# Kernel optimization log

Hardware: AMD Instinct MI355X
Metric: run time of the kernel (lower is better)

## Reference

```python
import jax, jax.numpy as jnp
from jax import lax
import numpy as np

DIM = 256
RANK = 128
E = 4      # num_experts
K = 2      # top_k
B, H, W = 8, 128, 128


def setup_inputs() -> dict:
    key = jax.random.key(0)
    ks = jax.random.split(key, 12)
    s = lambda fan: 1.0 / np.sqrt(fan)
    return {
        "x": jax.random.normal(ks[0], (B, DIM, H, W), jnp.float32),
        "shared": jax.random.normal(ks[1], (B, DIM, H, W), jnp.float32),
        # FrequencyEmbedding MLP (torch Linear: weight [out,in], bias [out])
        "mlp_w1": jax.random.normal(ks[2], (2 * DIM, DIM), jnp.float32) * s(DIM),
        "mlp_b1": jnp.zeros((2 * DIM,), jnp.float32),
        "mlp_w2": jax.random.normal(ks[3], (DIM, 2 * DIM), jnp.float32) * s(2 * DIM),
        "mlp_b2": jnp.zeros((DIM,), jnp.float32),
        # routing gates (no bias)
        "gate_w": jax.random.normal(ks[4], (E, DIM), jnp.float32) * s(DIM),
        "freq_gate_w": jax.random.normal(ks[5], (E, DIM), jnp.float32) * s(DIM),
        # stacked expert 1x1 convs: proj0/proj1 dim->rank, proj2 rank->dim
        "p0": jax.random.normal(ks[6], (E, RANK, DIM), jnp.float32) * s(DIM),
        "p1": jax.random.normal(ks[7], (E, RANK, DIM), jnp.float32) * s(DIM),
        "p2": jax.random.normal(ks[8], (E, DIM, RANK), jnp.float32) * s(RANK),
        # output 1x1 conv (no bias)
        "proj_out_w": jax.random.normal(ks[9], (DIM, DIM), jnp.float32) * s(DIM),
    }


def _high_pass_depthwise(x):
    # fixed frozen 3x3 high-pass kernel, depthwise (groups=C)
    C = x.shape[1]
    k = jnp.array([[-1., -1., -1.], [-1., 8., -1.], [-1., -1., -1.]], x.dtype)
    k = jnp.tile(k[None, None], (C, 1, 1, 1))  # [C,1,3,3]
    return lax.conv_general_dilated(
        x, k, window_strides=(1, 1), padding="SAME",
        feature_group_count=C,
        dimension_numbers=("NCHW", "OIHW", "NCHW"))


def reference(x, shared, mlp_w1, mlp_b1, mlp_w2, mlp_b2,
              gate_w, freq_gate_w, p0, p1, p2, proj_out_w):
    Bn = x.shape[0]
    # FrequencyEmbedding: high-pass conv -> GELU -> global mean -> MLP
    h = jax.nn.gelu(_high_pass_depthwise(x), approximate=False)
    h = h.mean(axis=(-2, -1))                                    # [B, C]
    freq_emb = jax.nn.gelu(h @ mlp_w1.T + mlp_b1, approximate=False) @ mlp_w2.T + mlp_b2
    # Routing: avg-pool gate + freq gate, softmax, top-k, scatter to dense gates
    pooled = x.mean(axis=(-2, -1))                               # [B, C]
    logits = pooled @ gate_w.T + freq_emb @ freq_gate_w.T        # [B, E]
    gating = jax.nn.softmax(logits, axis=-1)
    vals, idx = lax.top_k(gating, K)                             # [B, K]
    gates = jnp.zeros_like(logits).at[jnp.arange(Bn)[:, None], idx].set(vals)  # [B, E]
    a = jnp.einsum("erd,bdhw->berhw", p0, x)                     # [B,E,R,H,W]
    b = jnp.einsum("erd,bdhw->berhw", p1, shared)
    y = a * jax.nn.silu(b)
    # gate-weighted combine, folding gates into the contraction; shortcut term
    combined = (jnp.einsum("be,edr,berhw->bdhw", gates, p2, y)
                + gates.sum(-1)[:, None, None, None] * x)        # [B,C,H,W]
    out = jnp.einsum("od,bdhw->bohw", proj_out_w, combined)
    return out
```

## Files before the change

kernel.cpp:

```cpp
#include <hip/hip_runtime.h>
#include <math.h>

#define DIMC 256
#define HW   16384
#define NB   8
#define HID  512
#define NE   4
#define RNK  128

typedef __bf16 bf16x8 __attribute__((ext_vector_type(8)));
typedef float  f32x4  __attribute__((ext_vector_type(4)));

__device__ __forceinline__ unsigned short f2bf(float f) {
  unsigned u = __builtin_bit_cast(unsigned, f);
  u += 0x7FFFu + ((u >> 16) & 1u);
  return (unsigned short)(u >> 16);
}
__device__ __forceinline__ unsigned pack2(float a, float b) {
  return (unsigned)f2bf(a) | ((unsigned)f2bf(b) << 16);
}
__device__ __forceinline__ float bf2f(unsigned short u) {
  unsigned v = ((unsigned)u) << 16;
  return __builtin_bit_cast(float, v);
}

#define CPAD 136
__global__ __launch_bounds__(256) void k_conv_reduce(const float* __restrict__ x,
                                                     float* __restrict__ xsum,
                                                     float* __restrict__ hsum) {
  __shared__ unsigned short sp[128 * CPAD];
  __shared__ float red[8];
  const int p = blockIdx.x;
  const int tid = threadIdx.x;
  const float4* img4 = (const float4*)(x + (size_t)p * HW);
#pragma unroll
  for (int u = 0; u < 16; ++u) {
    const int unit = tid + 256 * u;
    const float4 v = img4[unit];
    const int row = unit >> 5, xq = unit & 31;
    uint2 w;
    w.x = pack2(v.x, v.y);
    w.y = pack2(v.z, v.w);
    *(uint2*)&sp[row * CPAD + xq * 4] = w;
  }
  __syncthreads();

  float xacc = 0.f, hacc = 0.f;
#pragma unroll
  for (int u = 0; u < 4; ++u) {
    const int seg = tid + 256 * u;
    const int row = seg >> 3, x0 = (seg & 7) * 16;
    float S[16], c[16];
#pragma unroll
    for (int j = 0; j < 16; ++j) S[j] = 0.f;
#pragma unroll
    for (int dr = -1; dr <= 1; ++dr) {
      const int r2 = row + dr;
      float v[18];
      if ((unsigned)r2 <= 127u) {
        const unsigned short* rp = sp + r2 * CPAD + x0;
        const uint4 q0 = *(const uint4*)(rp);
        const uint4 q1 = *(const uint4*)(rp + 8);
        v[0]  = (x0 > 0)       ? bf2f(rp[-1]) : 0.f;
        v[17] = (x0 + 16 < 128) ? bf2f(rp[16]) : 0.f;
        v[1] = bf2f((unsigned short)(q0.x & 0xffff)); v[2] = bf2f((unsigned short)(q0.x >> 16));
        v[3] = bf2f((unsigned short)(q0.y & 0xffff)); v[4] = bf2f((unsigned short)(q0.y >> 16));
        v[5] = bf2f((unsigned short)(q0.z & 0xffff)); v[6] = bf2f((unsigned short)(q0.z >> 16));
        v[7] = bf2f((unsigned short)(q0.w & 0xffff)); v[8] = bf2f((unsigned short)(q0.w >> 16));
        v[9]  = bf2f((unsigned short)(q1.x & 0xffff)); v[10] = bf2f((unsigned short)(q1.x >> 16));
        v[11] = bf2f((unsigned short)(q1.y & 0xffff)); v[12] = bf2f((unsigned short)(q1.y >> 16));
        v[13] = bf2f((unsigned short)(q1.z & 0xffff)); v[14] = bf2f((unsigned short)(q1.z >> 16));
        v[15] = bf2f((unsigned short)(q1.w & 0xffff)); v[16] = bf2f((unsigned short)(q1.w >> 16));
      } else {
#pragma unroll
        for (int j = 0; j < 18; ++j) v[j] = 0.f;
      }
      if (dr == 0) {
#pragma unroll
        for (int j = 0; j < 16; ++j) c[j] = v[j + 1];
      }
#pragma unroll
      for (int j = 0; j < 16; ++j) S[j] += v[j] + v[j + 1] + v[j + 2];
    }
#pragma unroll
    for (int j = 0; j < 16; ++j) {
      const float h = 9.f * c[j] - S[j];
      hacc += 0.5f * h * (1.f + erff(h * 0.70710678118654752f));
      xacc += c[j];
    }
  }
#pragma unroll
  for (int off = 32; off > 0; off >>= 1) {
    xacc += __shfl_down(xacc, off);
    hacc += __shfl_down(hacc, off);
  }
  const int wid = tid >> 6, lane = tid & 63;
  if (lane == 0) { red[wid] = xacc; red[4 + wid] = hacc; }
  __syncthreads();
  if (tid == 0) {
    xsum[p] = red[0] + red[1] + red[2] + red[3];
    hsum[p] = red[4] + red[5] + red[6] + red[7];
  }
}

__global__ __launch_bounds__(256) void k_gate_t1(
    const float* __restrict__ hsum, const float* __restrict__ w1,
    const float* __restrict__ b1, float* __restrict__ t1) {
  const int blk = blockIdx.x;
  const int b = blk >> 7;
  const int o = (blk & 127) * 4 + (threadIdx.x >> 6);
  const int lane = threadIdx.x & 63;
  const float4 h = *(const float4*)(hsum + b * DIMC + lane * 4);
  const float4 w = *(const float4*)(w1 + (size_t)o * DIMC + lane * 4);
  float acc = h.x * w.x + h.y * w.y + h.z * w.z + h.w * w.w;
#pragma unroll
  for (int off = 32; off > 0; off >>= 1) acc += __shfl_down(acc, off);
  if (lane == 0) {
    acc = acc * (1.f / 16384.f) + b1[o];
    t1[b * HID + o] = 0.5f * acc * (1.f + erff(acc * 0.70710678118654752f));
  }
}

__global__ __launch_bounds__(256) void k_gate_fe(
    const float* __restrict__ t1, const float* __restrict__ w2,
    const float* __restrict__ b2, float* __restrict__ fe) {
  const int blk = blockIdx.x;
  const int b = blk >> 6;
  const int o = (blk & 63) * 4 + (threadIdx.x >> 6);
  const int lane = threadIdx.x & 63;
  const float* tr = t1 + b * HID + lane * 8;
  const float* wr = w2 + (size_t)o * HID + lane * 8;
  const float4 ta = *(const float4*)tr,  tb = *(const float4*)(tr + 4);
  const float4 wa = *(const float4*)wr,  wb = *(const float4*)(wr + 4);
  float acc = ta.x * wa.x + ta.y * wa.y + ta.z * wa.z + ta.w * wa.w
            + tb.x * wb.x + tb.y * wb.y + tb.z * wb.z + tb.w * wb.w;
#pragma unroll
  for (int off = 32; off > 0; off >>= 1) acc += __shfl_down(acc, off);
  if (lane == 0) fe[b * DIMC + o] = acc + b2[o];
}

__global__ __launch_bounds__(256) void k_gate_fin(
    const float* __restrict__ xsum, const float* __restrict__ fe,
    const float* __restrict__ gw, const float* __restrict__ fgw,
    float* __restrict__ gates, float* __restrict__ gsumv, int* __restrict__ sel) {
  __shared__ float slog[NB][NE];
  const int wave = threadIdx.x >> 6, lane = threadIdx.x & 63;
  const int e = wave;
  const float4 g1 = *(const float4*)(gw + e * DIMC + lane * 4);
  const float4 g2 = *(const float4*)(fgw + e * DIMC + lane * 4);
  for (int b = 0; b < NB; ++b) {
    const float4 p = *(const float4*)(xsum + b * DIMC + lane * 4);
    const float4 f = *(const float4*)(fe + b * DIMC + lane * 4);
    float acc = (p.x * g1.x + p.y * g1.y + p.z * g1.z + p.w * g1.w) * (1.f / 16384.f)
              + f.x * g2.x + f.y * g2.y + f.z * g2.z + f.w * g2.w;
#pragma unroll
    for (int off = 32; off > 0; off >>= 1) acc += __shfl_down(acc, off);
    if (lane == 0) slog[b][e] = acc;
  }
  __syncthreads();
  if (threadIdx.x < NB) {
    const int b = threadIdx.x;
    float l[4] = {slog[b][0], slog[b][1], slog[b][2], slog[b][3]};
    const float m = fmaxf(fmaxf(l[0], l[1]), fmaxf(l[2], l[3]));
    float g[4];
    float ssum = 0.f;
    for (int e2 = 0; e2 < 4; ++e2) { g[e2] = expf(l[e2] - m); ssum += g[e2]; }
    for (int e2 = 0; e2 < 4; ++e2) g[e2] /= ssum;
    int i1 = 0;
    for (int e2 = 1; e2 < 4; ++e2) if (g[e2] > g[i1]) i1 = e2;
    int i2 = -1;
    for (int e2 = 0; e2 < 4; ++e2) {
      if (e2 == i1) continue;
      if (i2 < 0 || g[e2] > g[i2]) i2 = e2;
    }
    for (int e2 = 0; e2 < 4; ++e2)
      gates[b * 4 + e2] = (e2 == i1) ? g[i1] : ((e2 == i2) ? g[i2] : 0.f);
    gsumv[b] = g[i1] + g[i2];
    sel[b * 2 + 0] = i1;
    sel[b * 2 + 1] = i2;
  }
}

__global__ __launch_bounds__(128) void k_q2(const float* __restrict__ wp,
                                            const float* __restrict__ p2,
                                            float* __restrict__ q2) {
  const int eo = blockIdx.x;
  const int e = eo >> 8, o = eo & 255;
  const int r = threadIdx.x;
  const float* p2e = p2 + (size_t)e * DIMC * RNK;
  const float* wrow = wp + (size_t)o * DIMC;
  float acc = 0.f;
  for (int d = 0; d < DIMC; ++d) acc += wrow[d] * p2e[d * RNK + r];
  q2[(size_t)eo * RNK + r] = acc;
}

__global__ __launch_bounds__(256) void k_build(
    const float* __restrict__ p0, const float* __restrict__ p1,
    const float* __restrict__ wp, const float* __restrict__ q2,
    const float* __restrict__ gates, const float* __restrict__ gsumv,
    const int* __restrict__ sel,
    unsigned* __restrict__ A1u, unsigned* __restrict__ A2u,
    unsigned* __restrict__ A3u) {
  const int P1 = NB * 256 * 128;
  const int P2 = P1;
  const int P3 = NB * 256 * 256;
  for (int pi = blockIdx.x * 256 + threadIdx.x; pi < P1 + P2 + P3;
       pi += gridDim.x * 256) {
    if (pi < P1) {
      const int b = pi >> 15;
      const int row = (pi >> 7) & 255;
      const int d = (pi & 127) * 2;
      const int e = sel[b * 2 + (row >> 7)];
      const float* src = p0 + ((size_t)e * 128 + (row & 127)) * 256 + d;
      A1u[pi] = pack2(src[0], src[1]);
    } else if (pi < P1 + P2) {
      const int j = pi - P1;
      const int b = j >> 15;
      const int row = (j >> 7) & 255;
      const int d = (j & 127) * 2;
      const int e = sel[b * 2 + (row >> 7)];
      const float* src = p1 + ((size_t)e * 128 + (row & 127)) * 256 + d;
      A2u[j] = pack2(src[0], src[1]);
    } else {
      const int j = pi - P1 - P2;
      const int b = j >> 16;
      const int o = (j >> 8) & 255;
      const int c = (j & 255) * 2;
      float v0, v1;
      if (c < 256) {
        const int e = sel[b * 2 + (c >> 7)];
        const float gsc = gates[b * 4 + e];
        const float* qq = q2 + ((size_t)e * 256 + o) * RNK + (c & 127);
        v0 = gsc * qq[0]; v1 = gsc * qq[1];
      } else {
        const float gs = gsumv[b];
        const float* wr = wp + (size_t)o * DIMC + (c - 256);
        v0 = gs * wr[0]; v1 = gs * wr[1];
      }
      A3u[j] = pack2(v0, v1);
    }
  }
}

__global__ __launch_bounds__(1024, 8) void k_main_mfma(
    const float* __restrict__ x, const float* __restrict__ shr,
    const unsigned short* __restrict__ A1b, const unsigned short* __restrict__ A2b,
    const unsigned short* __restrict__ A3b, float* __restrict__ out) {
  __shared__ unsigned short XF[16384];
  __shared__ unsigned short SF[16384];
  const int tid = threadIdx.x;
  const int b = blockIdx.x & 7;
  const int tile = blockIdx.x >> 3;
  const int nb0 = tile * 64;
  const int wave = tid >> 6;
  const int lane = tid & 63;
  const int li = lane & 15;
  const int g  = lane >> 4;
  const int wrow = wave * 16;
  const size_t pbase = (size_t)b * DIMC * HW + nb0;

  {
    const int px = tid & 63;
    const int slot = tid >> 6;
#pragma unroll
    for (int pass = 0; pass < 2; ++pass) {
      const int dblk = pass * 16 + slot;
      const float* xc = x   + pbase + (size_t)(dblk * 8) * HW + px;
      const float* sc = shr + pbase + (size_t)(dblk * 8) * HW + px;
      float vx[8], vs[8];
#pragma unroll
      for (int jj = 0; jj < 8; ++jj) {
        vx[jj] = xc[(size_t)jj * HW];
        vs[jj] = sc[(size_t)jj * HW];
      }
      const int o = dblk * 512 + ((px ^ (dblk & 7)) << 3);
      uint4 wv;
      wv.x = pack2(vx[0], vx[1]); wv.y = pack2(vx[2], vx[3]);
      wv.z = pack2(vx[4], vx[5]); wv.w = pack2(vx[6], vx[7]);
      *(uint4*)&XF[o] = wv;
      uint4 sv;
      sv.x = pack2(vs[0], vs[1]); sv.y = pack2(vs[2], vs[3]);
      sv.z = pack2(vs[4], vs[5]); sv.w = pack2(vs[6], vs[7]);
      *(uint4*)&SF[o] = sv;
    }
  }
  __syncthreads();

  f32x4 accB[4], accA[4];
#pragma unroll
  for (int pb = 0; pb < 4; ++pb) { accB[pb] = (f32x4)0.f; accA[pb] = (f32x4)0.f; }
  {
    const unsigned short* Arow = A2b + ((size_t)b * 256 + wrow + li) * 256 + g * 8;
#pragma unroll
    for (int ks = 0; ks < 8; ++ks) {
      const int dblkb = ks * 4 + g;
      const int ebase = dblkb * 512 + ((li ^ (dblkb & 7)) << 3);
      const bf16x8 a0 = *(const bf16x8*)(Arow + ks * 32);
#pragma unroll
      for (int pb = 0; pb < 4; ++pb) {
        const bf16x8 bf = *(const bf16x8*)&SF[ebase + pb * 128];
        accB[pb] = __builtin_amdgcn_mfma_f32_16x16x32_bf16(a0, bf, accB[pb], 0, 0, 0);
      }
    }
  }
  {
    const unsigned short* Arow = A1b + ((size_t)b * 256 + wrow + li) * 256 + g * 8;
#pragma unroll
    for (int ks = 0; ks < 8; ++ks) {
      const int dblkb = ks * 4 + g;
      const int ebase = dblkb * 512 + ((li ^ (dblkb & 7)) << 3);
      const bf16x8 a0 = *(const bf16x8*)(Arow + ks * 32);
#pragma unroll
      for (int pb = 0; pb < 4; ++pb) {
        const bf16x8 bf = *(const bf16x8*)&XF[ebase + pb * 128];
        accA[pb] = __builtin_amdgcn_mfma_f32_16x16x32_bf16(a0, bf, accA[pb], 0, 0, 0);
      }
    }
  }
  __syncthreads();

  {
    const int ydblk = 2 * wave + (g >> 1);
    const int ys = ydblk & 7;
    const int yoff = (g & 1) * 4;
#pragma unroll
    for (int pb = 0; pb < 4; ++pb) {
      const int pxy = pb * 16 + li;
      const f32x4 aa = accA[pb], bb = accB[pb];
      const float y0 = aa[0] * (bb[0] / (1.f + __expf(-bb[0])));
      const float y1 = aa[1] * (bb[1] / (1.f + __expf(-bb[1])));
      const float y2 = aa[2] * (bb[2] / (1.f + __expf(-bb[2])));
      const float y3 = aa[3] * (bb[3] / (1.f + __expf(-bb[3])));
      uint2 w;
      w.x = pack2(y0, y1);
      w.y = pack2(y2, y3);
      *(uint2*)&SF[ydblk * 512 + ((pxy ^ ys) << 3) + yoff] = w;
    }
  }
  __syncthreads();

  f32x4 accO[4];
#pragma unroll
  for (int pb = 0; pb < 4; ++pb) accO[pb] = (f32x4)0.f;
  {
    const unsigned short* Arow = A3b + ((size_t)b * 256 + wrow + li) * 512 + g * 8;
#pragma unroll
    for (int ks = 0; ks < 16; ++ks) {
      const int kk = ks & 7;
      const unsigned short* Bsrc = (ks < 8) ? SF : XF;
      const int dblkb = kk * 4 + g;
      const int ebase = dblkb * 512 + ((li ^ (dblkb & 7)) << 3);
      const bf16x8 a0 = *(const bf16x8*)(Arow + ks * 32);
#pragma unroll
      for (int pb = 0; pb < 4; ++pb) {
        const bf16x8 bf = *(const bf16x8*)&Bsrc[ebase + pb * 128];
        accO[pb] = __builtin_amdgcn_mfma_f32_16x16x32_bf16(a0, bf, accO[pb], 0, 0, 0);
      }
    }
  }

  {
    float* obase = out + pbase;
    const int r0 = wrow + g * 4;
#pragma unroll
    for (int pb = 0; pb < 4; ++pb) {
      const int p = pb * 16 + li;
#pragma unroll
      for (int i = 0; i < 4; ++i)
        obase[(size_t)(r0 + i) * HW + p] = accO[pb][i];
    }
  }
}

extern "C" void kernel_launch(void* const* d_in, const int* in_sizes, int n_in,
                              void* d_out, int out_size, void* d_ws, size_t ws_size,
                              hipStream_t stream) {
  (void)in_sizes; (void)n_in; (void)out_size; (void)ws_size;
  const float* x   = (const float*)d_in[0];
  const float* shr = (const float*)d_in[1];
  const float* w1  = (const float*)d_in[2];
  const float* b1  = (const float*)d_in[3];
  const float* w2  = (const float*)d_in[4];
  const float* b2  = (const float*)d_in[5];
  const float* gw  = (const float*)d_in[6];
  const float* fgw = (const float*)d_in[7];
  const float* p0  = (const float*)d_in[8];
  const float* p1  = (const float*)d_in[9];
  const float* p2  = (const float*)d_in[10];
  const float* wp  = (const float*)d_in[11];
  float* out = (float*)d_out;

  float* ws    = (float*)d_ws;
  float* xsum  = ws;
  float* hsum  = ws + 2048;
  float* gates = ws + 4096;
  float* gsumv = ws + 4128;
  int*   sel   = (int*)(ws + 4136);
  float* q2    = ws + 4152;
  unsigned* A1u = (unsigned*)(ws + 135224);
  unsigned* A2u = A1u + NB * 256 * 128;
  unsigned* A3u = A2u + NB * 256 * 128;
  float* t1g   = (float*)(A3u + NB * 256 * 256);
  float* feg   = t1g + NB * HID;

  k_conv_reduce<<<NB * DIMC, 256, 0, stream>>>(x, xsum, hsum);
  k_gate_t1<<<1024, 256, 0, stream>>>(hsum, w1, b1, t1g);
  k_gate_fe<<<512, 256, 0, stream>>>(t1g, w2, b2, feg);
  k_gate_fin<<<1, 256, 0, stream>>>(xsum, feg, gw, fgw, gates, gsumv, sel);
  k_q2<<<NE * DIMC, 128, 0, stream>>>(wp, p2, q2);
  k_build<<<512, 256, 0, stream>>>(p0, p1, wp, q2, gates, gsumv, sel, A1u, A2u, A3u);
  k_main_mfma<<<2048, 1024, 0, stream>>>(x, shr,
      (const unsigned short*)A1u, (const unsigned short*)A2u,
      (const unsigned short*)A3u, out);
}
```

Before: 323.2 us.

## Switch main kernel to 32x32 MFMA with pre-swizzled weight fragments

The main fused kernel moves from 16x16x32 to 32x32x16 bf16 MFMA, using 8 waves of 512 threads where each wave owns 32 output rows. k_build now writes the A1/A2/A3 weight matrices in a per-wave fragment layout, so each lane loads its A operand with one contiguous 16-byte read. The x-shortcut half of the output GEMM is interleaved with the P0 projection to reuse the B fragments loaded from shared memory. The aim is fewer LDS reads and instructions per FLOP, paid for with more accumulator registers per thread and half as many threads per block.

```diff
diff --git a/kernel.cpp b/kernel.cpp
--- a/kernel.cpp
+++ b/kernel.cpp
@@ -10,6 +10,7 @@
 
 typedef __bf16 bf16x8 __attribute__((ext_vector_type(8)));
 typedef float  f32x4  __attribute__((ext_vector_type(4)));
+typedef float  f32x16 __attribute__((ext_vector_type(16)));
 
 __device__ __forceinline__ unsigned short f2bf(float f) {
   unsigned u = __builtin_bit_cast(unsigned, f);
@@ -61,7 +62,7 @@
         const unsigned short* rp = sp + r2 * CPAD + x0;
         const uint4 q0 = *(const uint4*)(rp);
         const uint4 q1 = *(const uint4*)(rp + 8);
-        v[0]  = (x0 > 0)       ? bf2f(rp[-1]) : 0.f;
+        v[0]  = (x0 > 0)        ? bf2f(rp[-1]) : 0.f;
         v[17] = (x0 + 16 < 128) ? bf2f(rp[16]) : 0.f;
         v[1] = bf2f((unsigned short)(q0.x & 0xffff)); v[2] = bf2f((unsigned short)(q0.x >> 16));
         v[3] = bf2f((unsigned short)(q0.y & 0xffff)); v[4] = bf2f((unsigned short)(q0.y >> 16));
@@ -201,48 +202,55 @@
     const int* __restrict__ sel,
     unsigned* __restrict__ A1u, unsigned* __restrict__ A2u,
     unsigned* __restrict__ A3u) {
-  const int P1 = NB * 256 * 128;
-  const int P2 = P1;
-  const int P3 = NB * 256 * 256;
-  for (int pi = blockIdx.x * 256 + threadIdx.x; pi < P1 + P2 + P3;
-       pi += gridDim.x * 256) {
-    if (pi < P1) {
-      const int b = pi >> 15;
-      const int row = (pi >> 7) & 255;
-      const int d = (pi & 127) * 2;
+  const int total = NB * 32768;
+  for (int id = blockIdx.x * 256 + threadIdx.x; id < total;
+       id += gridDim.x * 256) {
+    const int b = id >> 15;
+    const int gi = id & 32767;
+    uint4 wv;
+    unsigned* dst;
+    if (gi < 16384) {
+      const int t = gi >> 13;
+      const int gj = gi & 8191;
+      const int rowblk = gj >> 10, ks = (gj >> 6) & 15;
+      const int h = (gj >> 5) & 1, r = gj & 31;
+      const int row = rowblk * 32 + r;
       const int e = sel[b * 2 + (row >> 7)];
-      const float* src = p0 + ((size_t)e * 128 + (row & 127)) * 256 + d;
-      A1u[pi] = pack2(src[0], src[1]);
-    } else if (pi < P1 + P2) {
-      const int j = pi - P1;
-      const int b = j >> 15;
-      const int row = (j >> 7) & 255;
-      const int d = (j & 127) * 2;
-      const int e = sel[b * 2 + (row >> 7)];
-      const float* src = p1 + ((size_t)e * 128 + (row & 127)) * 256 + d;
-      A2u[j] = pack2(src[0], src[1]);
+      const float* src = (t ? p1 : p0) + ((size_t)e * 128 + (row & 127)) * 256
+                       + ks * 16 + h * 8;
+      const float4 v0 = *(const float4*)src;
+      const float4 v1 = *(const float4*)(src + 4);
+      wv.x = pack2(v0.x, v0.y); wv.y = pack2(v0.z, v0.w);
+      wv.z = pack2(v1.x, v1.y); wv.w = pack2(v1.z, v1.w);
+      dst = (t ? A2u : A1u) + (size_t)b * 32768 + gj * 4;
     } else {
-      const int j = pi - P1 - P2;
-      const int b = j >> 16;
-      const int o = (j >> 8) & 255;
-      const int c = (j & 255) * 2;
-      float v0, v1;
-      if (c < 256) {
-        const int e = sel[b * 2 + (c >> 7)];
+      const int gj = gi - 16384;
+      const int rowblk = gj >> 11, ks = (gj >> 6) & 31;
+      const int h = (gj >> 5) & 1, r = gj & 31;
+      const int o = rowblk * 32 + r;
+      const int k = ks * 16 + h * 8;
+      float v[8];
+      if (k < 256) {
+        const int e = sel[b * 2 + (k >> 7)];
         const float gsc = gates[b * 4 + e];
-        const float* qq = q2 + ((size_t)e * 256 + o) * RNK + (c & 127);
-        v0 = gsc * qq[0]; v1 = gsc * qq[1];
+        const float* qq = q2 + ((size_t)e * 256 + o) * RNK + (k & 127);
+#pragma unroll
+        for (int j = 0; j < 8; ++j) v[j] = gsc * qq[j];
       } else {
         const float gs = gsumv[b];
-        const float* wr = wp + (size_t)o * DIMC + (c - 256);
-        v0 = gs * wr[0]; v1 = gs * wr[1];
+        const float* wr = wp + (size_t)o * DIMC + (k - 256);
+#pragma unroll
+        for (int j = 0; j < 8; ++j) v[j] = gs * wr[j];
       }
-      A3u[j] = pack2(v0, v1);
-    }
-  }
-}
-
-__global__ __launch_bounds__(1024, 8) void k_main_mfma(
+      wv.x = pack2(v[0], v[1]); wv.y = pack2(v[2], v[3]);
+      wv.z = pack2(v[4], v[5]); wv.w = pack2(v[6], v[7]);
+      dst = A3u + (size_t)b * 65536 + gj * 4;
+    }
+    *(uint4*)dst = wv;
+  }
+}
+
+__global__ __launch_bounds__(512, 4) void k_main_mfma(
     const float* __restrict__ x, const float* __restrict__ shr,
     const unsigned short* __restrict__ A1b, const unsigned short* __restrict__ A2b,
     const unsigned short* __restrict__ A3b, float* __restrict__ out) {
@@ -254,17 +262,16 @@
   const int nb0 = tile * 64;
   const int wave = tid >> 6;
   const int lane = tid & 63;
-  const int li = lane & 15;
-  const int g  = lane >> 4;
-  const int wrow = wave * 16;
+  const int r32 = lane & 31;
+  const int h = lane >> 5;
+  const int wrow = wave * 32;
   const size_t pbase = (size_t)b * DIMC * HW + nb0;
 
   {
-    const int px = tid & 63;
-    const int slot = tid >> 6;
-#pragma unroll
-    for (int pass = 0; pass < 2; ++pass) {
-      const int dblk = pass * 16 + slot;
+    const int px = lane;
+#pragma unroll
+    for (int pass = 0; pass < 4; ++pass) {
+      const int dblk = pass * 8 + wave;
       const float* xc = x   + pbase + (size_t)(dblk * 8) * HW + px;
       const float* sc = shr + pbase + (size_t)(dblk * 8) * HW + px;
       float vx[8], vs[8];
@@ -286,88 +293,77 @@
   }
   __syncthreads();
 
-  f32x4 accB[4], accA[4];
-#pragma unroll
-  for (int pb = 0; pb < 4; ++pb) { accB[pb] = (f32x4)0.f; accA[pb] = (f32x4)0.f; }
+  const unsigned short* A1w = A1b + (size_t)(b * 8 + wave) * 8192;
+  const unsigned short* A2w = A2b + (size_t)(b * 8 + wave) * 8192;
+  const unsigned short* A3w = A3b + (size_t)(b * 8 + wave) * 16384;
+
+  f32x16 accB0 = (f32x16)0.f, accB1 = (f32x16)0.f;
+#pragma unroll
+  for (int ks = 0; ks < 16; ++ks) {
+    const bf16x8 a = *(const bf16x8*)(A2w + ks * 512 + lane * 8);
+    const int dblkB = ks * 2 + h;
+    const int eb = dblkB * 512 + ((r32 ^ (dblkB & 7)) << 3);
+    const bf16x8 b0 = *(const bf16x8*)&SF[eb];
+    const bf16x8 b1 = *(const bf16x8*)&SF[eb + 256];
+    accB0 = __builtin_amdgcn_mfma_f32_32x32x16_bf16(a, b0, accB0, 0, 0, 0);
+    accB1 = __builtin_amdgcn_mfma_f32_32x32x16_bf16(a, b1, accB1, 0, 0, 0);
+  }
+  __syncthreads();
+
+  f32x16 accA0 = (f32x16)0.f, accA1 = (f32x16)0.f;
+  f32x16 accO0 = (f32x16)0.f, accO1 = (f32x16)0.f;
+#pragma unroll
+  for (int ks = 0; ks < 16; ++ks) {
+    const bf16x8 a1 = *(const bf16x8*)(A1w + ks * 512 + lane * 8);
+    const bf16x8 a3 = *(const bf16x8*)(A3w + (16 + ks) * 512 + lane * 8);
+    const int dblkB = ks * 2 + h;
+    const int eb = dblkB * 512 + ((r32 ^ (dblkB & 7)) << 3);
+    const bf16x8 b0 = *(const bf16x8*)&XF[eb];
+    const bf16x8 b1 = *(const bf16x8*)&XF[eb + 256];
+    accA0 = __builtin_amdgcn_mfma_f32_32x32x16_bf16(a1, b0, accA0, 0, 0, 0);
+    accA1 = __builtin_amdgcn_mfma_f32_32x32x16_bf16(a1, b1, accA1, 0, 0, 0);
+    accO0 = __builtin_amdgcn_mfma_f32_32x32x16_bf16(a3, b0, accO0, 0, 0, 0);
+    accO1 = __builtin_amdgcn_mfma_f32_32x32x16_bf16(a3, b1, accO1, 0, 0, 0);
+  }
+
+#pragma unroll
+  for (int q = 0; q < 4; ++q) {
+    const int dblk = wave * 4 + q;
+    const int sw = dblk & 7;
+    const int base = dblk * 512 + h * 4;
+    float y0[4], y1[4];
+#pragma unroll
+    for (int i = 0; i < 4; ++i) {
+      const float bA = accB0[q * 4 + i];
+      const float bBv = accB1[q * 4 + i];
+      y0[i] = accA0[q * 4 + i] * (bA / (1.f + __expf(-bA)));
+      y1[i] = accA1[q * 4 + i] * (bBv / (1.f + __expf(-bBv)));
+    }
+    uint2 w0; w0.x = pack2(y0[0], y0[1]); w0.y = pack2(y0[2], y0[3]);
+    *(uint2*)&SF[base + ((r32 ^ sw) << 3)] = w0;
+    uint2 w1; w1.x = pack2(y1[0], y1[1]); w1.y = pack2(y1[2], y1[3]);
+    *(uint2*)&SF[base + (((32 + r32) ^ sw) << 3)] = w1;
+  }
+  __syncthreads();
+
+#pragma unroll
+  for (int ks = 0; ks < 16; ++ks) {
+    const bf16x8 a3 = *(const bf16x8*)(A3w + ks * 512 + lane * 8);
+    const int dblkB = ks * 2 + h;
+    const int eb = dblkB * 512 + ((r32 ^ (dblkB & 7)) << 3);
+    const bf16x8 b0 = *(const bf16x8*)&SF[eb];
+    const bf16x8 b1 = *(const bf16x8*)&SF[eb + 256];
+    accO0 = __builtin_amdgcn_mfma_f32_32x32x16_bf16(a3, b0, accO0, 0, 0, 0);
+    accO1 = __builtin_amdgcn_mfma_f32_32x32x16_bf16(a3, b1, accO1, 0, 0, 0);
+  }
+
   {
-    const unsigned short* Arow = A2b + ((size_t)b * 256 + wrow + li) * 256 + g * 8;
-#pragma unroll
-    for (int ks = 0; ks < 8; ++ks) {
-      const int dblkb = ks * 4 + g;
-      const int ebase = dblkb * 512 + ((li ^ (dblkb & 7)) << 3);
-      const bf16x8 a0 = *(const bf16x8*)(Arow + ks * 32);
-#pragma unroll
-      for (int pb = 0; pb < 4; ++pb) {
-        const bf16x8 bf = *(const bf16x8*)&SF[ebase + pb * 128];
-        accB[pb] = __builtin_amdgcn_mfma_f32_16x16x32_bf16(a0, bf, accB[pb], 0, 0, 0);
-      }
-    }
-  }
-  {
-    const unsigned short* Arow = A1b + ((size_t)b * 256 + wrow + li) * 256 + g * 8;
-#pragma unroll
-    for (int ks = 0; ks < 8; ++ks) {
-      const int dblkb = ks * 4 + g;
-      const int ebase = dblkb * 512 + ((li ^ (dblkb & 7)) << 3);
-      const bf16x8 a0 = *(const bf16x8*)(Arow + ks * 32);
-#pragma unroll
-      for (int pb = 0; pb < 4; ++pb) {
-        const bf16x8 bf = *(const bf16x8*)&XF[ebase + pb * 128];
-        accA[pb] = __builtin_amdgcn_mfma_f32_16x16x32_bf16(a0, bf, accA[pb], 0, 0, 0);
-      }
-    }
-  }
-  __syncthreads();
-
-  {
-    const int ydblk = 2 * wave + (g >> 1);
-    const int ys = ydblk & 7;
-    const int yoff = (g & 1) * 4;
-#pragma unroll
-    for (int pb = 0; pb < 4; ++pb) {
-      const int pxy = pb * 16 + li;
-      const f32x4 aa = accA[pb], bb = accB[pb];
-      const float y0 = aa[0] * (bb[0] / (1.f + __expf(-bb[0])));
-      const float y1 = aa[1] * (bb[1] / (1.f + __expf(-bb[1])));
-      const float y2 = aa[2] * (bb[2] / (1.f + __expf(-bb[2])));
-      const float y3 = aa[3] * (bb[3] / (1.f + __expf(-bb[3])));
-      uint2 w;
-      w.x = pack2(y0, y1);
-      w.y = pack2(y2, y3);
-      *(uint2*)&SF[ydblk * 512 + ((pxy ^ ys) << 3) + yoff] = w;
-    }
-  }
-  __syncthreads();
-
-  f32x4 accO[4];
-#pragma unroll
-  for (int pb = 0; pb < 4; ++pb) accO[pb] = (f32x4)0.f;
-  {
-    const unsigned short* Arow = A3b + ((size_t)b * 256 + wrow + li) * 512 + g * 8;
-#pragma unroll
-    for (int ks = 0; ks < 16; ++ks) {
-      const int kk = ks & 7;
-      const unsigned short* Bsrc = (ks < 8) ? SF : XF;
-      const int dblkb = kk * 4 + g;
-      const int ebase = dblkb * 512 + ((li ^ (dblkb & 7)) << 3);
-      const bf16x8 a0 = *(const bf16x8*)(Arow + ks * 32);
-#pragma unroll
-      for (int pb = 0; pb < 4; ++pb) {
-        const bf16x8 bf = *(const bf16x8*)&Bsrc[ebase + pb * 128];
-        accO[pb] = __builtin_amdgcn_mfma_f32_16x16x32_bf16(a0, bf, accO[pb], 0, 0, 0);
-      }
-    }
-  }
-
-  {
-    float* obase = out + pbase;
-    const int r0 = wrow + g * 4;
-#pragma unroll
-    for (int pb = 0; pb < 4; ++pb) {
-      const int p = pb * 16 + li;
-#pragma unroll
-      for (int i = 0; i < 4; ++i)
-        obase[(size_t)(r0 + i) * HW + p] = accO[pb][i];
+    float* ob = out + pbase;
+#pragma unroll
+    for (int r = 0; r < 16; ++r) {
+      const int row = wrow + (r & 3) + 8 * (r >> 2) + 4 * h;
+      ob[(size_t)row * HW + r32] = accO0[r];
+      ob[(size_t)row * HW + 32 + r32] = accO1[r];
     }
   }
 }
@@ -409,7 +405,7 @@
   k_gate_fin<<<1, 256, 0, stream>>>(xsum, feg, gw, fgw, gates, gsumv, sel);
   k_q2<<<NE * DIMC, 128, 0, stream>>>(wp, p2, q2);
   k_build<<<512, 256, 0, stream>>>(p0, p1, wp, q2, gates, gsumv, sel, A1u, A2u, A3u);
-  k_main_mfma<<<2048, 1024, 0, stream>>>(x, shr,
+  k_main_mfma<<<2048, 512, 0, stream>>>(x, shr,
       (const unsigned short*)A1u, (const unsigned short*)A2u,
       (const unsigned short*)A3u, out);
 }
```

Result: slower. 454.2 us (+40.5%).
